# Kernel optimization log

Hardware: AMD Instinct MI355X
Metric: run time of the kernel (lower is better)

Reference implementation:

```python
import jax, jax.numpy as jnp
import numpy as np

B, S, D_IN, D_OUT = 4, 2048, 1024, 1024

def setup_inputs() -> dict:
    key = jax.random.key(0)
    ks = jax.random.split(key, 6)
    s = 1.0 / np.sqrt(D_IN)
    return {
        "inputs": jax.random.normal(ks[0], (B, S, D_IN), dtype=jnp.float32),
        "Wq": jax.random.normal(ks[1], (D_IN, D_OUT), dtype=jnp.float32) * s,
        "Wk": jax.random.normal(ks[2], (D_IN, D_OUT), dtype=jnp.float32) * s,
        "Wv": jax.random.normal(ks[3], (D_IN, D_OUT), dtype=jnp.float32) * s,
        "Wo": jax.random.normal(ks[4], (D_OUT, D_OUT), dtype=jnp.float32) * (1.0 / np.sqrt(D_OUT)),
        "bo": jax.random.normal(ks[5], (D_OUT,), dtype=jnp.float32) * 0.01,
    }

def reference(inputs, Wq, Wk, Wv, Wo, bo):
    # QKV projections (no bias, matching qkv_bias=False)
    q = inputs @ Wq  # [B,S,D]
    k = inputs @ Wk
    v = inputs @ Wv
    # naive full attention: scores [B,S,S]
    scores = jnp.einsum('bqd,bkd->bqk', q, k) / jnp.sqrt(jnp.asarray(k.shape[-1], q.dtype))
    attn = jax.nn.softmax(scores, axis=-1)
    out = jnp.einsum('bqk,bkd->bqd', attn, v)
    return out @ Wo + bo
```

## Files before the change

### kernel.cpp

```cpp
#include <hip/hip_runtime.h>
#include <hip/hip_bf16.h>
#include <cstdint>

typedef __attribute__((ext_vector_type(8))) __bf16 bf16x8;
typedef __attribute__((ext_vector_type(4))) float  f32x4;

__device__ __forceinline__ unsigned short f2bf(float x) {
    union { float f; unsigned u; } v; v.f = x;
    unsigned r = v.u + 0x7fffu + ((v.u >> 16) & 1u);
    return (unsigned short)(r >> 16);
}
__device__ __forceinline__ unsigned pack2bf(float a, float b) {
    return (unsigned)f2bf(a) | ((unsigned)f2bf(b) << 16);
}

__device__ __forceinline__ void gld_lds16(const unsigned short* g, unsigned short* l) {
    __builtin_amdgcn_global_load_lds(
        (const __attribute__((address_space(1))) unsigned int*)g,
        (__attribute__((address_space(3))) unsigned int*)l,
        16, 0, 0);
}

__global__ void cvt_kernel(const float* __restrict__ in, unsigned short* __restrict__ out, int n4) {
    int i = blockIdx.x * blockDim.x + threadIdx.x;
    if (i < n4) {
        float4 f = ((const float4*)in)[i];
        ushort4 o;
        o.x = f2bf(f.x); o.y = f2bf(f.y); o.z = f2bf(f.z); o.w = f2bf(f.w);
        ((ushort4*)out)[i] = o;
    }
}

__global__ void wpack_kernel(const float* __restrict__ W, unsigned short* __restrict__ out) {
    int tid  = threadIdx.x;
    int lane = tid & 63;
    int chunk = blockIdx.x * 4 + (tid >> 6);
    int nt = chunk >> 5, k32 = chunk & 31;
    int r = lane & 15, q = lane >> 4;
    const float* src = W + (size_t)(k32*32 + q*8) * 1024 + nt*16 + r;
    unsigned o[4];
#pragma unroll
    for (int i = 0; i < 4; i++)
        o[i] = pack2bf(src[(size_t)(2*i) * 1024], src[(size_t)(2*i+1) * 1024]);
    *(uint4*)(out + (size_t)chunk * 512 + lane * 8) = make_uint4(o[0], o[1], o[2], o[3]);
}

__global__ void softmax_kernel(unsigned short* __restrict__ S) {
    const size_t row = blockIdx.x;
    unsigned short* p = S + row * 2048;
    const int tid = threadIdx.x;
    const int wave = tid >> 6, lane = tid & 63;

    uint4 raw = ((const uint4*)p)[tid];
    unsigned u[4] = {raw.x, raw.y, raw.z, raw.w};
    float x[8];
#pragma unroll
    for (int i = 0; i < 4; i++) {
        x[2*i]   = __uint_as_float(u[i] << 16);
        x[2*i+1] = __uint_as_float(u[i] & 0xffff0000u);
    }
    float m = x[0];
#pragma unroll
    for (int i = 1; i < 8; i++) m = fmaxf(m, x[i]);
#pragma unroll
    for (int off = 32; off >= 1; off >>= 1) m = fmaxf(m, __shfl_xor(m, off, 64));
    __shared__ float sm[4], ss[4];
    if (lane == 0) sm[wave] = m;
    __syncthreads();
    m = fmaxf(fmaxf(sm[0], sm[1]), fmaxf(sm[2], sm[3]));

    float e[8], s = 0.f;
#pragma unroll
    for (int i = 0; i < 8; i++) { e[i] = __expf(x[i] - m); s += e[i]; }
#pragma unroll
    for (int off = 32; off >= 1; off >>= 1) s += __shfl_xor(s, off, 64);
    if (lane == 0) ss[wave] = s;
    __syncthreads();
    s = ss[0] + ss[1] + ss[2] + ss[3];
    float inv = 1.0f / s;

    unsigned o[4];
#pragma unroll
    for (int i = 0; i < 4; i++)
        o[i] = pack2bf(e[2*i] * inv, e[2*i+1] * inv);
    ((uint4*)p)[tid] = make_uint4(o[0], o[1], o[2], o[3]);
}

template<int EPI>
__global__ __launch_bounds__(512, 2)
void gemm8p(const unsigned short* __restrict__ A, const unsigned short* __restrict__ Bpk,
            void* __restrict__ C, unsigned short* __restrict__ Ck, unsigned short* __restrict__ Cv,
            int lda, int ldc, int KS, int ns, float scale,
            long long sA, long long sB, long long sC)
{
    __shared__ __align__(16) char smem[131072];

    const int tid  = threadIdx.x;
    const int lane = tid & 63;
    const int wave = tid >> 6;
    const int bz = blockIdx.z;
    A   += (size_t)bz * sA;
    Bpk += (size_t)bz * sB;

    const int gx = gridDim.x;
    int lin = blockIdx.y * gx + blockIdx.x;
    int cpx = (gx * gridDim.y) >> 3;
    int swz = (lin & 7) * cpx + (lin >> 3);
    const int bm = (swz / gx) * 256;
    const int bn = (swz % gx) * 256;

    const int wm = (wave & 1) * 128;
    const int wn = (wave >> 1) * 64;
    const int ln15 = lane & 15;
    const int quad = lane >> 4;
    const int fko = (quad ^ ((ln15 >> 1) & 3)) * 8;

    const int srow = tid >> 2;
    const int scol = ((tid & 3) ^ ((tid >> 3) & 3)) * 8;
    const unsigned short* paU = A + (size_t)(bm + srow) * lda + scol;
    const unsigned short* paL = A + (size_t)(bm + 128 + srow) * lda + scol;
    const unsigned short* pb0 = Bpk + (size_t)((bn >> 4) + (tid >> 6)) * KS * 512 + lane * 8;
    const long long pbstep = (long long)8 * KS * 512;

    f32x4 acc[8][4];
#pragma unroll
    for (int i = 0; i < 8; i++)
#pragma unroll
        for (int j = 0; j < 4; j++) acc[i][j] = (f32x4){0.f, 0.f, 0.f, 0.f};

    auto stageA = [&](int buf, int t, int k) {
        char* d = smem + buf * 32768 + k * 16384 + tid * 16;
        const unsigned short* s = paU + t * 64 + k * 32;
        gld_lds16(s, (unsigned short*)d);
        gld_lds16(paL + t * 64 + k * 32, (unsigned short*)(d + 8192));
    };
    auto stageB = [&](int buf, int t, int k) {
        char* d = smem + 65536 + buf * 32768 + k * 16384 + (tid >> 6) * 1024 + lane * 16;
        const unsigned short* s = pb0 + (size_t)(2 * t + k) * 512;
        gld_lds16(s, (unsigned short*)d);
        gld_lds16(s + pbstep, (unsigned short*)(d + 8192));
    };
    auto dsread12 = [&](int buf, int k, bf16x8* af, bf16x8* bfr) {
        const unsigned short* Ar = (const unsigned short*)(smem + buf * 32768 + k * 16384);
        const unsigned short* Br = (const unsigned short*)(smem + 65536 + buf * 32768 + k * 16384);
#pragma unroll
        for (int im = 0; im < 8; im++)
            af[im] = *(const bf16x8*)&Ar[(wm + (im >> 2) * 64 + (im & 3) * 16 + ln15) * 32 + fko];
#pragma unroll
        for (int j = 0; j < 4; j++)
            bfr[j] = *(const bf16x8*)&Br[((wn >> 4) + j) * 512 + lane * 8];
    };
    auto mfma32 = [&](const bf16x8* af, const bf16x8* bfr) {
        __builtin_amdgcn_s_setprio(1);
#pragma unroll
        for (int im = 0; im < 8; im++)
#pragma unroll
            for (int j = 0; j < 4; j++)
                acc[im][j] = __builtin_amdgcn_mfma_f32_16x16x32_bf16(
                    af[im], bfr[j], acc[im][j], 0, 0, 0);
        __builtin_amdgcn_s_setprio(0);
    };

#define BAR   __builtin_amdgcn_s_barrier()
#define FEN   asm volatile("" ::: "memory")
#define VM4   asm volatile("s_waitcnt vmcnt(4)" ::: "memory")

    stageB(0, 0, 0); stageA(0, 0, 0); stageB(0, 0, 1); stageA(0, 0, 1);
    VM4; BAR; FEN;

    bf16x8 af[8], bfr[4];
    for (int t = 0; t < ns; ++t) {
        const int buf = t & 1, nb = buf ^ 1;
        const int tn = (t + 1 < ns) ? t + 1 : 0;
        dsread12(buf, 0, af, bfr);
        stageB(nb, tn, 0); stageA(nb, tn, 0);
        mfma32(af, bfr);
        VM4;
        BAR; FEN;
        dsread12(buf, 1, af, bfr);
        stageB(nb, tn, 1); stageA(nb, tn, 1);
        mfma32(af, bfr);
        VM4;
        BAR; FEN;
    }
#undef BAR
#undef FEN
#undef VM4

    if (EPI == 1) {
        __syncthreads();
        float* ep = (float*)(smem + wave * 4352);
        unsigned short* Co = (unsigned short*)C + (size_t)bz * sC;
#pragma unroll
        for (int im = 0; im < 8; im++) {
            int mrow = (im >> 2) * 64 + (im & 3) * 16;
#pragma unroll
            for (int j = 0; j < 4; j++)
#pragma unroll
                for (int r = 0; r < 4; r++)
                    ep[(quad*4 + r) * 68 + j*16 + ln15] = acc[im][j][r] * scale;
            __builtin_amdgcn_s_waitcnt(0);
#pragma unroll
            for (int pp = 0; pp < 2; pp++) {
                int lrow = pp*8 + (lane >> 3);
                int col0 = (lane & 7) * 8;
                float4 lo = *(const float4*)&ep[lrow * 68 + col0];
                float4 hi = *(const float4*)&ep[lrow * 68 + col0 + 4];
                uint4 o;
                o.x = pack2bf(lo.x, lo.y); o.y = pack2bf(lo.z, lo.w);
                o.z = pack2bf(hi.x, hi.y); o.w = pack2bf(hi.z, hi.w);
                *(uint4*)&Co[(size_t)(bm + wm + mrow + lrow) * ldc + bn + wn + col0] = o;
            }
            __builtin_amdgcn_s_waitcnt(0);
        }
    } else {
        __syncthreads();
        float* ep = (float*)(smem + wave * 8704);
        const int region = bn >> 10;
#pragma unroll
        for (int g = 0; g < 4; g++) {
#pragma unroll
            for (int ii = 0; ii < 2; ii++) {
                int im = g*2 + ii;
#pragma unroll
                for (int j = 0; j < 4; j++)
#pragma unroll
                    for (int r = 0; r < 4; r++)
                        ep[(ii*16 + quad*4 + r) * 68 + j*16 + ln15] = acc[im][j][r] * scale;
            }
            __builtin_amdgcn_s_waitcnt(0);
            const int mrow0 = bm + wm + g*32;
            if (region == 0) {
                unsigned short* Q = (unsigned short*)C;
#pragma unroll
                for (int pp = 0; pp < 4; pp++) {
                    int lrow = pp*8 + (lane >> 3);
                    int col0 = (lane & 7) * 8;
                    float4 lo = *(const float4*)&ep[lrow * 68 + col0];
                    float4 hi = *(const float4*)&ep[lrow * 68 + col0 + 4];
                    uint4 o;
                    o.x = pack2bf(lo.x, lo.y); o.y = pack2bf(lo.z, lo.w);
                    o.z = pack2bf(hi.x, hi.y); o.w = pack2bf(hi.z, hi.w);
                    *(uint4*)&Q[(size_t)(mrow0 + lrow) * ldc + bn + wn + col0] = o;
                }
            } else if (region == 1) {
#pragma unroll
                for (int mt = 0; mt < 2; mt++)
#pragma unroll
                    for (int c = 0; c < 2; c++) {
                        float4 f0 = *(const float4*)&ep[(mt*16 + ln15) * 68 + c*32 + quad*8];
                        float4 f1 = *(const float4*)&ep[(mt*16 + ln15) * 68 + c*32 + quad*8 + 4];
                        uint4 o;
                        o.x = pack2bf(f0.x, f0.y); o.y = pack2bf(f0.z, f0.w);
                        o.z = pack2bf(f1.x, f1.y); o.w = pack2bf(f1.z, f1.w);
                        int cid = ((mrow0 + mt*16) >> 4) * 32 + ((bn - 1024 + wn + c*32) >> 5);
                        *(uint4*)(Ck + (size_t)cid * 512 + lane * 8) = o;
                    }
            } else {
                int s32 = mrow0 >> 5;
#pragma unroll
                for (int dt = 0; dt < 4; dt++) {
                    float v[8];
#pragma unroll
                    for (int e = 0; e < 8; e++)
                        v[e] = ep[(quad*8 + e) * 68 + dt*16 + ln15];
                    uint4 o;
                    o.x = pack2bf(v[0], v[1]); o.y = pack2bf(v[2], v[3]);
                    o.z = pack2bf(v[4], v[5]); o.w = pack2bf(v[6], v[7]);
                    int cid = (((bn - 2048 + wn) >> 4) + dt) * 256 + s32;
                    *(uint4*)(Cv + (size_t)cid * 512 + lane * 8) = o;
                }
            }
            __builtin_amdgcn_s_waitcnt(0);
        }
    }
}

template<int EPI>
__global__ __launch_bounds__(512, 2)
void gemm_pk(const unsigned short* __restrict__ A, const unsigned short* __restrict__ Bpk,
             void* __restrict__ C, unsigned short* __restrict__ Ck, unsigned short* __restrict__ Cv,
             const float* __restrict__ bias,
             int lda, int ldc, int KS, int ns, float scale,
             long long sA, long long sB, long long sC)
{
    __shared__ __align__(16) char smem[98304];

    const int tid  = threadIdx.x;
    const int lane = tid & 63;
    const int wave = tid >> 6;
    const int bz = blockIdx.z;
    A   += (size_t)bz * sA;
    Bpk += (size_t)bz * sB;

    const int gx = gridDim.x;
    int lin = blockIdx.y * gx + blockIdx.x;
    int cpx = (gx * gridDim.y) >> 3;
    int swz = (lin & 7) * cpx + (lin >> 3);
    const int bm = (swz / gx) * 256;
    const int bn = (swz % gx) * 128;

    const int srow = tid >> 2;
    const int scol = ((tid & 3) ^ ((tid >> 3) & 3)) * 8;
    const unsigned short* pa0 = A + (size_t)(bm + srow) * lda + scol;
    const unsigned short* pa1 = pa0 + 32;
    const unsigned short* pa2 = A + (size_t)(bm + 128 + srow) * lda + scol;
    const unsigned short* pa3 = pa2 + 32;

    const int wm = (wave & 3) * 64;
    const int wn = (wave >> 2) * 64;
    const int ln15 = lane & 15;
    const int quad = lane >> 4;
    const int fko = (quad ^ ((ln15 >> 1) & 3)) * 8;
    const int rbase = (wm >> 7) * 4096 + (wm & 127) * 32;
    const int ldsoff = tid * 16;

    const unsigned short* pb[4];
#pragma unroll
    for (int j = 0; j < 4; j++)
        pb[j] = Bpk + (size_t)(((bn + wn + j*16) >> 4) * KS) * 512 + lane * 8;

    f32x4 acc[4][4];
#pragma unroll
    for (int i = 0; i < 4; i++)
#pragma unroll
        for (int j = 0; j < 4; j++) acc[i][j] = (f32x4){0.f, 0.f, 0.f, 0.f};

    auto dma = [&](int buf) {
        char* base = smem + buf * 32768;
        gld_lds16(pa0, (unsigned short*)(base + ldsoff));
        gld_lds16(pa2, (unsigned short*)(base + 8192  + ldsoff));
        gld_lds16(pa1, (unsigned short*)(base + 16384 + ldsoff));
        gld_lds16(pa3, (unsigned short*)(base + 24576 + ldsoff));
        pa0 += 64; pa1 += 64; pa2 += 64; pa3 += 64;
    };
    auto loadB = [&](bf16x8* br) {
#pragma unroll
        for (int j = 0; j < 4; j++) {
            br[j]     = *(const bf16x8*)(pb[j]);
            br[4 + j] = *(const bf16x8*)(pb[j] + 512);
            pb[j] += 1024;
        }
    };
    auto phase = [&](const unsigned short* As, int t, const bf16x8* br) {
        bf16x8 af[4];
#pragma unroll
        for (int i = 0; i < 4; i++)
            af[i] = *(const bf16x8*)&As[t*8192 + rbase + i*512 + ln15*32 + fko];
        __builtin_amdgcn_s_setprio(1);
#pragma unroll
        for (int i = 0; i < 4; i++)
#pragma unroll
            for (int j = 0; j < 4; j++)
                acc[i][j] = __builtin_amdgcn_mfma_f32_16x16x32_bf16(
                    af[i], br[t*4 + j], acc[i][j], 0, 0, 0);
        __builtin_amdgcn_s_setprio(0);
    };

#define SB __builtin_amdgcn_sched_barrier(0)
    bf16x8 b0[8], b1[8];
    SB; dma(0); SB; loadB(b0); SB; dma(1); SB;

    int p = 0;
    for (int it = 0; it < ns; it += 2) {
        const unsigned short* As0 = (const unsigned short*)(smem + p * 32768);
        int p1 = p + 1; if (p1 >= 3) p1 -= 3;
        int q0 = p + 2; if (q0 >= 3) q0 -= 3;
        const unsigned short* As1 = (const unsigned short*)(smem + p1 * 32768);
        const bool more = (it + 2 < ns);

        asm volatile("s_waitcnt vmcnt(12)" ::: "memory");
        SB; __builtin_amdgcn_s_barrier(); SB;
        loadB(b1); SB;
        phase(As0, 0, b0);
        __builtin_amdgcn_s_barrier(); SB;
        if (more) { dma(q0); SB; }
        phase(As0, 1, b0);

        if (more) { asm volatile("s_waitcnt vmcnt(12)" ::: "memory"); }
        else      { asm volatile("s_waitcnt vmcnt(8)"  ::: "memory"); }
        SB; __builtin_amdgcn_s_barrier(); SB;
        if (more) { loadB(b0); SB; }
        phase(As1, 0, b1);
        __builtin_amdgcn_s_barrier(); SB;
        if (it + 3 < ns) { dma(p); SB; }
        phase(As1, 1, b1);

        p = q0;
    }
#undef SB

    if (EPI == 0) {
        float bval[4];
#pragma unroll
        for (int j = 0; j < 4; j++) bval[j] = bias[bn + wn + j*16 + ln15];
        float* Co = (float*)C + (size_t)bz * sC;
#pragma unroll
        for (int i = 0; i < 4; i++) {
            int r0 = bm + wm + i*16 + quad*4;
#pragma unroll
            for (int j = 0; j < 4; j++) {
                int c = bn + wn + j*16 + ln15;
#pragma unroll
                for (int r = 0; r < 4; r++)
                    Co[(size_t)(r0 + r) * ldc + c] = acc[i][j][r] * scale + bval[j];
            }
        }
    } else if (EPI == 1) {
        __syncthreads();
        float* ep = (float*)(smem + wave * 4352);
        unsigned short* Co = (unsigned short*)C + (size_t)bz * sC;
#pragma unroll
        for (int i = 0; i < 4; i++) {
#pragma unroll
            for (int j = 0; j < 4; j++)
#pragma unroll
                for (int r = 0; r < 4; r++)
                    ep[(quad*4 + r) * 68 + j*16 + ln15] = acc[i][j][r] * scale;
            __builtin_amdgcn_s_waitcnt(0);
#pragma unroll
            for (int pp = 0; pp < 2; pp++) {
                int lrow = pp*8 + (lane >> 3);
                int col0 = (lane & 7) * 8;
                float4 lo = *(const float4*)&ep[lrow * 68 + col0];
                float4 hi = *(const float4*)&ep[lrow * 68 + col0 + 4];
                uint4 o;
                o.x = pack2bf(lo.x, lo.y); o.y = pack2bf(lo.z, lo.w);
                o.z = pack2bf(hi.x, hi.y); o.w = pack2bf(hi.z, hi.w);
                *(uint4*)&Co[(size_t)(bm + wm + i*16 + lrow) * ldc + bn + wn + col0] = o;
            }
            __builtin_amdgcn_s_waitcnt(0);
        }
    }
}

extern "C" void kernel_launch(void* const* d_in, const int* in_sizes, int n_in,
                              void* d_out, int out_size, void* d_ws, size_t ws_size,
                              hipStream_t stream) {
    const float* X  = (const float*)d_in[0];
    const float* Wq = (const float*)d_in[1];
    const float* Wk = (const float*)d_in[2];
    const float* Wv = (const float*)d_in[3];
    const float* Wo = (const float*)d_in[4];
    const float* bo = (const float*)d_in[5];
    float* out = (float*)d_out;

    size_t off = 0;
    auto alloc = [&](size_t bytes) {
        void* p = (char*)d_ws + off;
        off += (bytes + 255) & ~(size_t)255;
        return p;
    };
    unsigned short* Xbf  = (unsigned short*)alloc(8192ull * 1024 * 2);
    unsigned short* Wpk  = (unsigned short*)alloc(192ull * 32 * 512 * 2);
    unsigned short* Wopk = (unsigned short*)alloc(64ull * 32 * 512 * 2);
    unsigned short* Qrm  = (unsigned short*)alloc(8192ull * 1024 * 2);
    unsigned short* Kpk  = (unsigned short*)alloc(512ull * 32 * 512 * 2);
    unsigned short* Vpk  = (unsigned short*)alloc(64ull * 256 * 512 * 2);
    unsigned short* Sc   = (unsigned short*)alloc(4ull * 2048 * 2048 * 2);
    unsigned short* AO   = Xbf;

    cvt_kernel<<<(8192*1024/4 + 255)/256, 256, 0, stream>>>(X, Xbf, 8192*1024/4);
    wpack_kernel<<<512, 256, 0, stream>>>(Wq, Wpk);
    wpack_kernel<<<512, 256, 0, stream>>>(Wk, Wpk + 64*32*512);
    wpack_kernel<<<512, 256, 0, stream>>>(Wv, Wpk + 128*32*512);
    wpack_kernel<<<512, 256, 0, stream>>>(Wo, Wopk);

    gemm8p<2><<<dim3(3072/256, 8192/256, 1), 512, 0, stream>>>(
        Xbf, Wpk, Qrm, Kpk, Vpk, 1024, 1024, 32, 16, 1.0f, 0, 0, 0);

    gemm8p<1><<<dim3(2048/256, 2048/256, 4), 512, 0, stream>>>(
        Qrm, Kpk, Sc, nullptr, nullptr, 1024, 2048, 32, 16, 0.03125f,
        2048ll*1024, 128ll*32*512, 2048ll*2048);

    softmax_kernel<<<8192, 256, 0, stream>>>(Sc);

    gemm_pk<1><<<dim3(1024/128, 2048/256, 4), 512, 0, stream>>>(
        Sc, Vpk, AO, nullptr, nullptr, nullptr, 2048, 1024, 256, 32, 1.0f,
        2048ll*2048, 64ll*512, 2048ll*1024);

    gemm_pk<0><<<dim3(1024/128, 8192/256, 1), 512, 0, stream>>>(
        AO, Wopk, out, nullptr, nullptr, bo, 1024, 1024, 32, 16, 1.0f, 0, 0, 0);

    (void)n_in; (void)in_sizes; (void)out_size; (void)ws_size;
}
```

Baseline: 274.6 us.

## Triple-buffer A tiles and merge K sub-steps into one barrier per iteration

Shared memory grows to hold three A stages and two B stages. A is now prefetched two K-tiles ahead and B one ahead. Each iteration reads both K halves into separate fragment registers, runs all MFMAs, and then waits at a single barrier instead of two. The aim is to halve barrier stalls and hide more global-load latency, at the cost of doubled fragment registers (risking spills under the 512,2 launch bounds) and the full 160KB of LDS.

```diff
diff --git a/kernel.cpp b/kernel.cpp
--- a/kernel.cpp
+++ b/kernel.cpp
@@ -93,7 +93,7 @@
             int lda, int ldc, int KS, int ns, float scale,
             long long sA, long long sB, long long sC)
 {
-    __shared__ __align__(16) char smem[131072];
+    __shared__ __align__(16) char smem[163840];
 
     const int tid  = threadIdx.x;
     const int lane = tid & 63;
@@ -135,14 +135,14 @@
         gld_lds16(paL + t * 64 + k * 32, (unsigned short*)(d + 8192));
     };
     auto stageB = [&](int buf, int t, int k) {
-        char* d = smem + 65536 + buf * 32768 + k * 16384 + (tid >> 6) * 1024 + lane * 16;
+        char* d = smem + 98304 + buf * 32768 + k * 16384 + (tid >> 6) * 1024 + lane * 16;
         const unsigned short* s = pb0 + (size_t)(2 * t + k) * 512;
         gld_lds16(s, (unsigned short*)d);
         gld_lds16(s + pbstep, (unsigned short*)(d + 8192));
     };
-    auto dsread12 = [&](int buf, int k, bf16x8* af, bf16x8* bfr) {
-        const unsigned short* Ar = (const unsigned short*)(smem + buf * 32768 + k * 16384);
-        const unsigned short* Br = (const unsigned short*)(smem + 65536 + buf * 32768 + k * 16384);
+    auto dsread12 = [&](int abuf, int bbuf, int k, bf16x8* af, bf16x8* bfr) {
+        const unsigned short* Ar = (const unsigned short*)(smem + abuf * 32768 + k * 16384);
+        const unsigned short* Br = (const unsigned short*)(smem + 98304 + bbuf * 32768 + k * 16384);
 #pragma unroll
         for (int im = 0; im < 8; im++)
             af[im] = *(const bf16x8*)&Ar[(wm + (im >> 2) * 64 + (im & 3) * 16 + ln15) * 32 + fko];
@@ -165,23 +165,27 @@
 #define FEN   asm volatile("" ::: "memory")
 #define VM4   asm volatile("s_waitcnt vmcnt(4)" ::: "memory")
 
-    stageB(0, 0, 0); stageA(0, 0, 0); stageB(0, 0, 1); stageA(0, 0, 1);
+    stageA(0, 0, 0); stageA(0, 0, 1);
+    stageB(0, 0, 0); stageB(0, 0, 1);
+    stageA(1, 1, 0); stageA(1, 1, 1);
     VM4; BAR; FEN;
 
-    bf16x8 af[8], bfr[4];
+    bf16x8 af0[8], bfr0[4], af1[8], bfr1[4];
+    int abuf = 0;
     for (int t = 0; t < ns; ++t) {
-        const int buf = t & 1, nb = buf ^ 1;
-        const int tn = (t + 1 < ns) ? t + 1 : 0;
-        dsread12(buf, 0, af, bfr);
-        stageB(nb, tn, 0); stageA(nb, tn, 0);
-        mfma32(af, bfr);
+        const int bbuf = t & 1;
+        int tn1 = t + 1; if (tn1 >= ns) tn1 -= ns;
+        int tn2 = t + 2; if (tn2 >= ns) tn2 -= ns;
+        int ab2 = abuf + 2; if (ab2 >= 3) ab2 -= 3;
+        stageB(bbuf ^ 1, tn1, 0); stageB(bbuf ^ 1, tn1, 1);
+        stageA(ab2, tn2, 0); stageA(ab2, tn2, 1);
+        dsread12(abuf, bbuf, 0, af0, bfr0);
+        dsread12(abuf, bbuf, 1, af1, bfr1);
+        mfma32(af0, bfr0);
+        mfma32(af1, bfr1);
         VM4;
         BAR; FEN;
-        dsread12(buf, 1, af, bfr);
-        stageB(nb, tn, 1); stageA(nb, tn, 1);
-        mfma32(af, bfr);
-        VM4;
-        BAR; FEN;
+        ++abuf; if (abuf >= 3) abuf -= 3;
     }
 #undef BAR
 #undef FEN
```

After: 284.8 us. 1.04x slower.

## Fuse softmax into QK^T and PV GEMM epilogues, split V projection

Applied to the files above, without the earlier changes.

Removes the standalone softmax pass. The QK^T GEMM epilogue now writes exp(scores) directly and accumulates per-row sums with atomics into a zeroed buffer, and the PV GEMM epilogue divides by those row sums. The max subtraction is dropped, so the change relies on the score magnitudes staying small enough for exp not to overflow. The V projection moves out of the fused QKV GEMM into its own gemm_pk launch with a new epilogue (EPI 4), which shrinks the first GEMM grid and adds one launch.

```diff
diff --git a/kernel.cpp b/kernel.cpp
--- a/kernel.cpp
+++ b/kernel.cpp
@@ -31,6 +31,11 @@
     }
 }
 
+__global__ void zero_kernel(float* __restrict__ p, int n) {
+    int i = blockIdx.x * blockDim.x + threadIdx.x;
+    if (i < n) p[i] = 0.f;
+}
+
 __global__ void wpack_kernel(const float* __restrict__ W, unsigned short* __restrict__ out) {
     int tid  = threadIdx.x;
     int lane = tid & 63;
@@ -43,47 +48,6 @@
     for (int i = 0; i < 4; i++)
         o[i] = pack2bf(src[(size_t)(2*i) * 1024], src[(size_t)(2*i+1) * 1024]);
     *(uint4*)(out + (size_t)chunk * 512 + lane * 8) = make_uint4(o[0], o[1], o[2], o[3]);
-}
-
-__global__ void softmax_kernel(unsigned short* __restrict__ S) {
-    const size_t row = blockIdx.x;
-    unsigned short* p = S + row * 2048;
-    const int tid = threadIdx.x;
-    const int wave = tid >> 6, lane = tid & 63;
-
-    uint4 raw = ((const uint4*)p)[tid];
-    unsigned u[4] = {raw.x, raw.y, raw.z, raw.w};
-    float x[8];
-#pragma unroll
-    for (int i = 0; i < 4; i++) {
-        x[2*i]   = __uint_as_float(u[i] << 16);
-        x[2*i+1] = __uint_as_float(u[i] & 0xffff0000u);
-    }
-    float m = x[0];
-#pragma unroll
-    for (int i = 1; i < 8; i++) m = fmaxf(m, x[i]);
-#pragma unroll
-    for (int off = 32; off >= 1; off >>= 1) m = fmaxf(m, __shfl_xor(m, off, 64));
-    __shared__ float sm[4], ss[4];
-    if (lane == 0) sm[wave] = m;
-    __syncthreads();
-    m = fmaxf(fmaxf(sm[0], sm[1]), fmaxf(sm[2], sm[3]));
-
-    float e[8], s = 0.f;
-#pragma unroll
-    for (int i = 0; i < 8; i++) { e[i] = __expf(x[i] - m); s += e[i]; }
-#pragma unroll
-    for (int off = 32; off >= 1; off >>= 1) s += __shfl_xor(s, off, 64);
-    if (lane == 0) ss[wave] = s;
-    __syncthreads();
-    s = ss[0] + ss[1] + ss[2] + ss[3];
-    float inv = 1.0f / s;
-
-    unsigned o[4];
-#pragma unroll
-    for (int i = 0; i < 4; i++)
-        o[i] = pack2bf(e[2*i] * inv, e[2*i+1] * inv);
-    ((uint4*)p)[tid] = make_uint4(o[0], o[1], o[2], o[3]);
 }
 
 template<int EPI>
@@ -187,18 +151,42 @@
 #undef FEN
 #undef VM4
 
-    if (EPI == 1) {
+    if (EPI == 1 || EPI == 3) {
         __syncthreads();
         float* ep = (float*)(smem + wave * 4352);
         unsigned short* Co = (unsigned short*)C + (size_t)bz * sC;
+        float* rsb = (EPI == 3) ? ((float*)Ck + (size_t)bz * 2048) : nullptr;
 #pragma unroll
         for (int im = 0; im < 8; im++) {
             int mrow = (im >> 2) * 64 + (im & 3) * 16;
-#pragma unroll
-            for (int j = 0; j < 4; j++)
-#pragma unroll
-                for (int r = 0; r < 4; r++)
-                    ep[(quad*4 + r) * 68 + j*16 + ln15] = acc[im][j][r] * scale;
+            if (EPI == 3) {
+                float ev[4][4];
+                float psum[4] = {0.f, 0.f, 0.f, 0.f};
+#pragma unroll
+                for (int j = 0; j < 4; j++)
+#pragma unroll
+                    for (int r = 0; r < 4; r++) {
+                        ev[j][r] = __expf(acc[im][j][r] * scale);
+                        psum[r] += ev[j][r];
+                        ep[(quad*4 + r) * 68 + j*16 + ln15] = ev[j][r];
+                    }
+#pragma unroll
+                for (int r = 0; r < 4; r++) {
+                    float v = psum[r];
+                    v += __shfl_xor(v, 1, 64);
+                    v += __shfl_xor(v, 2, 64);
+                    v += __shfl_xor(v, 4, 64);
+                    v += __shfl_xor(v, 8, 64);
+                    if (ln15 == 0)
+                        atomicAdd(&rsb[bm + wm + mrow + quad*4 + r], v);
+                }
+            } else {
+#pragma unroll
+                for (int j = 0; j < 4; j++)
+#pragma unroll
+                    for (int r = 0; r < 4; r++)
+                        ep[(quad*4 + r) * 68 + j*16 + ln15] = acc[im][j][r] * scale;
+            }
             __builtin_amdgcn_s_waitcnt(0);
 #pragma unroll
             for (int pp = 0; pp < 2; pp++) {
@@ -243,7 +231,7 @@
                     o.z = pack2bf(hi.x, hi.y); o.w = pack2bf(hi.z, hi.w);
                     *(uint4*)&Q[(size_t)(mrow0 + lrow) * ldc + bn + wn + col0] = o;
                 }
-            } else if (region == 1) {
+            } else {
 #pragma unroll
                 for (int mt = 0; mt < 2; mt++)
 #pragma unroll
@@ -256,20 +244,6 @@
                         int cid = ((mrow0 + mt*16) >> 4) * 32 + ((bn - 1024 + wn + c*32) >> 5);
                         *(uint4*)(Ck + (size_t)cid * 512 + lane * 8) = o;
                     }
-            } else {
-                int s32 = mrow0 >> 5;
-#pragma unroll
-                for (int dt = 0; dt < 4; dt++) {
-                    float v[8];
-#pragma unroll
-                    for (int e = 0; e < 8; e++)
-                        v[e] = ep[(quad*8 + e) * 68 + dt*16 + ln15];
-                    uint4 o;
-                    o.x = pack2bf(v[0], v[1]); o.y = pack2bf(v[2], v[3]);
-                    o.z = pack2bf(v[4], v[5]); o.w = pack2bf(v[6], v[7]);
-                    int cid = (((bn - 2048 + wn) >> 4) + dt) * 256 + s32;
-                    *(uint4*)(Cv + (size_t)cid * 512 + lane * 8) = o;
-                }
             }
             __builtin_amdgcn_s_waitcnt(0);
         }
@@ -410,13 +384,18 @@
         __syncthreads();
         float* ep = (float*)(smem + wave * 4352);
         unsigned short* Co = (unsigned short*)C + (size_t)bz * sC;
+        const float* rsb = bias ? bias + (size_t)bz * 2048 : nullptr;
 #pragma unroll
         for (int i = 0; i < 4; i++) {
+            float sc[4];
+#pragma unroll
+            for (int r = 0; r < 4; r++)
+                sc[r] = rsb ? (1.0f / rsb[bm + wm + i*16 + quad*4 + r]) : scale;
 #pragma unroll
             for (int j = 0; j < 4; j++)
 #pragma unroll
                 for (int r = 0; r < 4; r++)
-                    ep[(quad*4 + r) * 68 + j*16 + ln15] = acc[i][j][r] * scale;
+                    ep[(quad*4 + r) * 68 + j*16 + ln15] = acc[i][j][r] * sc[r];
             __builtin_amdgcn_s_waitcnt(0);
 #pragma unroll
             for (int pp = 0; pp < 2; pp++) {
@@ -428,6 +407,37 @@
                 o.x = pack2bf(lo.x, lo.y); o.y = pack2bf(lo.z, lo.w);
                 o.z = pack2bf(hi.x, hi.y); o.w = pack2bf(hi.z, hi.w);
                 *(uint4*)&Co[(size_t)(bm + wm + i*16 + lrow) * ldc + bn + wn + col0] = o;
+            }
+            __builtin_amdgcn_s_waitcnt(0);
+        }
+    } else {
+        __syncthreads();
+        float* ep = (float*)(smem + wave * 8704);
+#pragma unroll
+        for (int g = 0; g < 2; g++) {
+#pragma unroll
+            for (int ii = 0; ii < 2; ii++) {
+                int i = g*2 + ii;
+#pragma unroll
+                for (int j = 0; j < 4; j++)
+#pragma unroll
+                    for (int r = 0; r < 4; r++)
+                        ep[(ii*16 + quad*4 + r) * 68 + j*16 + ln15] = acc[i][j][r];
+            }
+            __builtin_amdgcn_s_waitcnt(0);
+            const int mrow0 = bm + wm + g*32;
+            const int s32 = mrow0 >> 5;
+#pragma unroll
+            for (int dt = 0; dt < 4; dt++) {
+                float v[8];
+#pragma unroll
+                for (int e = 0; e < 8; e++)
+                    v[e] = ep[(quad*8 + e) * 68 + dt*16 + ln15];
+                uint4 o;
+                o.x = pack2bf(v[0], v[1]); o.y = pack2bf(v[2], v[3]);
+                o.z = pack2bf(v[4], v[5]); o.w = pack2bf(v[6], v[7]);
+                int cid = (((bn + wn) >> 4) + dt) * 256 + s32;
+                *(uint4*)(Cv + (size_t)cid * 512 + lane * 8) = o;
             }
             __builtin_amdgcn_s_waitcnt(0);
         }
@@ -458,25 +468,29 @@
     unsigned short* Kpk  = (unsigned short*)alloc(512ull * 32 * 512 * 2);
     unsigned short* Vpk  = (unsigned short*)alloc(64ull * 256 * 512 * 2);
     unsigned short* Sc   = (unsigned short*)alloc(4ull * 2048 * 2048 * 2);
+    float*          RS   = (float*)alloc(4ull * 2048 * 4);
     unsigned short* AO   = Xbf;
 
     cvt_kernel<<<(8192*1024/4 + 255)/256, 256, 0, stream>>>(X, Xbf, 8192*1024/4);
+    zero_kernel<<<(8192 + 255)/256, 256, 0, stream>>>(RS, 4*2048);
     wpack_kernel<<<512, 256, 0, stream>>>(Wq, Wpk);
     wpack_kernel<<<512, 256, 0, stream>>>(Wk, Wpk + 64*32*512);
     wpack_kernel<<<512, 256, 0, stream>>>(Wv, Wpk + 128*32*512);
     wpack_kernel<<<512, 256, 0, stream>>>(Wo, Wopk);
 
-    gemm8p<2><<<dim3(3072/256, 8192/256, 1), 512, 0, stream>>>(
-        Xbf, Wpk, Qrm, Kpk, Vpk, 1024, 1024, 32, 16, 1.0f, 0, 0, 0);
-
-    gemm8p<1><<<dim3(2048/256, 2048/256, 4), 512, 0, stream>>>(
-        Qrm, Kpk, Sc, nullptr, nullptr, 1024, 2048, 32, 16, 0.03125f,
+    gemm8p<2><<<dim3(2048/256, 8192/256, 1), 512, 0, stream>>>(
+        Xbf, Wpk, Qrm, Kpk, nullptr, 1024, 1024, 32, 16, 1.0f, 0, 0, 0);
+
+    gemm_pk<4><<<dim3(1024/128, 8192/256, 1), 512, 0, stream>>>(
+        Xbf, Wpk + 128*32*512, nullptr, nullptr, Vpk, nullptr,
+        1024, 0, 32, 16, 1.0f, 0, 0, 0);
+
+    gemm8p<3><<<dim3(2048/256, 2048/256, 4), 512, 0, stream>>>(
+        Qrm, Kpk, Sc, (unsigned short*)RS, nullptr, 1024, 2048, 32, 16, 0.03125f,
         2048ll*1024, 128ll*32*512, 2048ll*2048);
 
-    softmax_kernel<<<8192, 256, 0, stream>>>(Sc);
-
     gemm_pk<1><<<dim3(1024/128, 2048/256, 4), 512, 0, stream>>>(
-        Sc, Vpk, AO, nullptr, nullptr, nullptr, 2048, 1024, 256, 32, 1.0f,
+        Sc, Vpk, AO, nullptr, nullptr, RS, 2048, 1024, 256, 32, 1.0f,
         2048ll*2048, 64ll*512, 2048ll*1024);
 
     gemm_pk<0><<<dim3(1024/128, 8192/256, 1), 512, 0, stream>>>(
```

Measured after the change: 282.0 us. +2.7%, slower.
